# Performance work log

Hardware: AMD Instinct MI355X
Metric: run time of the kernel (lower is better)

## Reference

```python
import jax, jax.numpy as jnp
import numpy as np

B, N, D, H = 4, 2048, 512, 8
DH = D // H
EPS = 1e-6


def setup_inputs() -> dict:
    key = jax.random.key(0)
    ks = jax.random.split(key, 12)
    s = 1.0 / np.sqrt(D)
    return {
        "x": jax.random.normal(ks[0], (B, N, D), jnp.float32),
        "attn_bias": jax.random.normal(ks[1], (B, 1, N, N), jnp.float32),
        "Wq": jax.random.normal(ks[2], (D, D), jnp.float32) * s,
        "bq": jnp.zeros((D,), jnp.float32),
        "Wk": jax.random.normal(ks[3], (D, D), jnp.float32) * s,
        "bk": jnp.zeros((D,), jnp.float32),
        "Wv": jax.random.normal(ks[4], (D, D), jnp.float32) * s,
        "bv": jnp.zeros((D,), jnp.float32),
        "Wo": jax.random.normal(ks[5], (D, D), jnp.float32) * s,
        "bo": jnp.zeros((D,), jnp.float32),
        "q_gamma": jnp.ones((DH,), jnp.float32),
        "q_beta": jnp.zeros((DH,), jnp.float32),
        "k_gamma": jnp.ones((DH,), jnp.float32),
        "k_beta": jnp.zeros((DH,), jnp.float32),
    }


def _layernorm(x, gamma, beta):
    mu = jnp.mean(x, axis=-1, keepdims=True)
    var = jnp.var(x, axis=-1, keepdims=True)
    return (x - mu) * jax.lax.rsqrt(var + EPS) * gamma + beta


def reference(x, attn_bias, Wq, bq, Wk, bk, Wv, bv, Wo, bo,
              q_gamma, q_beta, k_gamma, k_beta):
    b, n, d = x.shape
    # project and split heads: (B, H, N, DH)
    def heads(W, bias):
        return (x @ W.T + bias).reshape(b, n, H, DH).transpose(0, 2, 1, 3)
    q = heads(Wq, bq)
    k = heads(Wk, bk)
    v = heads(Wv, bv)
    q = _layernorm(q, q_gamma, q_beta)
    k = _layernorm(k, k_gamma, k_beta)
    scores = jnp.einsum('bhqd,bhkd->bhqk', q, k) / np.sqrt(DH)
    scores = scores + attn_bias  # (B,1,N,N) broadcasts over heads
    attn = jax.nn.softmax(scores, axis=-1)
    out = jnp.einsum('bhqk,bhkd->bhqd', attn, v)
    out = out.transpose(0, 2, 1, 3).reshape(b, n, d)
    return out @ Wo.T + bo
```

## Files before the change

### kernel.cpp

```cpp
#include <hip/hip_runtime.h>

typedef __attribute__((ext_vector_type(8))) short short8;
typedef __attribute__((ext_vector_type(4))) float f32x4;
typedef __attribute__((ext_vector_type(4))) int i32x4;
typedef __attribute__((ext_vector_type(4))) unsigned short u16x4;
typedef __attribute__((ext_vector_type(8))) unsigned short u16x8;
typedef __attribute__((ext_vector_type(2))) unsigned int u32x2;

#define B_  4
#define N_  2048
#define D_  512
#define H_  8
#define DH_ 64
#define M_  (B_ * N_)

__device__ __forceinline__ unsigned short f2bf(float f) {
    union { float f; unsigned u; } un; un.f = f;
    unsigned r = un.u + 0x7FFFu + ((un.u >> 16) & 1u);
    return (unsigned short)(r >> 16);
}
__device__ __forceinline__ unsigned packbf(float lo, float hi) {
    union { float f; unsigned u; } a, b;
    a.f = lo; b.f = hi;
    return __builtin_amdgcn_perm(b.u + 0x8000u, a.u + 0x8000u, 0x07060302u);
}
__device__ __forceinline__ float lo16f(unsigned u) {
    union { unsigned u; float f; } un; un.u = u << 16; return un.f;
}
__device__ __forceinline__ float hi16f(unsigned u) {
    union { unsigned u; float f; } un; un.u = u & 0xFFFF0000u; return un.f;
}
__device__ __forceinline__ float exp2fast(float x) {
#if __has_builtin(__builtin_amdgcn_exp2f)
    return __builtin_amdgcn_exp2f(x);
#else
    float r; asm("v_exp_f32 %0, %1" : "=v"(r) : "v"(x)); return r;
#endif
}

typedef __attribute__((address_space(1))) const void gvoid;
typedef __attribute__((address_space(3))) void svoid;
__device__ __forceinline__ void load16_lds(const void* g, void* s) {
    __builtin_amdgcn_global_load_lds((gvoid*)g, (svoid*)s, 16, 0, 0);
}

__global__ __launch_bounds__(256) void cvt_x(const float* __restrict__ src,
                                             unsigned short* __restrict__ dst) {
    const int i = (blockIdx.x * 256 + threadIdx.x) * 4;
    f32x4 v = *(const f32x4*)(src + i);
    u16x4 o;
    o[0] = f2bf(v[0]); o[1] = f2bf(v[1]); o[2] = f2bf(v[2]); o[3] = f2bf(v[3]);
    *(u16x4*)(dst + i) = o;
}

__global__ __launch_bounds__(256) void cvt_bias(const float* __restrict__ src,
                                                unsigned short* __restrict__ dst) {
    const size_t i = ((size_t)blockIdx.x * 256 + threadIdx.x) * 8;
    const int kv = (int)(i & 2047);
    const int q  = (int)((i >> 11) & 2047);
    const int b  = (int)(i >> 22);
    const float L2E = 1.4426950408889634f;
    f32x4 v0 = *(const f32x4*)(src + i);
    f32x4 v1 = *(const f32x4*)(src + i + 4);
    u16x8 o;
    o[0] = f2bf(v0[0] * L2E); o[1] = f2bf(v0[1] * L2E);
    o[2] = f2bf(v0[2] * L2E); o[3] = f2bf(v0[3] * L2E);
    o[4] = f2bf(v1[0] * L2E); o[5] = f2bf(v1[1] * L2E);
    o[6] = f2bf(v1[2] * L2E); o[7] = f2bf(v1[3] * L2E);
    const size_t oi = ((((size_t)b * 64 + (q >> 5)) * 32 + (kv >> 6)) * 32 + (q & 31)) * 64 + (kv & 63);
    *(u16x8*)(dst + oi) = o;
}

__global__ __launch_bounds__(256) void cvt_w(const float* __restrict__ W0,
                                             const float* __restrict__ W1,
                                             const float* __restrict__ W2,
                                             const float* __restrict__ W3,
                                             unsigned short* __restrict__ dst) {
    const int sel = blockIdx.y;
    const float* src = (sel == 0) ? W0 : (sel == 1) ? W1 : (sel == 2) ? W2 : W3;
    unsigned short* d = dst + (size_t)sel * D_ * D_;
    const int i = (blockIdx.x * 256 + threadIdx.x) * 4;
    f32x4 v = *(const f32x4*)(src + i);
    u16x4 o;
    o[0] = f2bf(v[0]); o[1] = f2bf(v[1]); o[2] = f2bf(v[2]); o[3] = f2bf(v[3]);
    *(u16x4*)(d + i) = o;
}

template <bool F32OUT, bool LNF>
__global__ __launch_bounds__(256, 2) void gemm_nt(
    const unsigned short* __restrict__ A,
    const unsigned short* __restrict__ W,
    const float* __restrict__ Bv0,
    const float* __restrict__ Bv1,
    const float* __restrict__ Bv2,
    const float* __restrict__ g0, const float* __restrict__ be0,
    const float* __restrict__ g1, const float* __restrict__ be1,
    unsigned short* __restrict__ outb,
    float* __restrict__ outf)
{
    const int mt = blockIdx.x;
    const int nt = blockIdx.y;
    const int sel = nt >> 2;
    const unsigned short* Wp = W + (size_t)sel * D_ * D_;
    const float* Bv = (sel == 0) ? Bv0 : (sel == 1) ? Bv1 : Bv2;
    const int n0 = (nt & 3) * 128;

    __shared__ __align__(16) unsigned short As[128 * 32];
    __shared__ __align__(16) unsigned short Bs[128 * 32];

    const int tid = threadIdx.x;
    const int w   = tid >> 6;
    const int l   = tid & 63;
    const int l15 = l & 15;
    const int qd  = l >> 4;
    const int wr  = w >> 1;
    const int wc  = w & 1;

    int srow[2], scol[2];
#pragma unroll
    for (int c = 0; c < 2; ++c) {
        const int g   = (w * 2 + c) * 64 + l;
        const int row = g >> 2;
        srow[c] = row;
        scol[c] = ((g & 3) ^ (row & 3)) * 8;
    }

    f32x4 acc[4][4];
#pragma unroll
    for (int i = 0; i < 4; ++i)
#pragma unroll
        for (int j = 0; j < 4; ++j)
            acc[i][j] = (f32x4){0.f, 0.f, 0.f, 0.f};

    const int swz = qd ^ (l15 & 3);

    for (int k0 = 0; k0 < D_; k0 += 32) {
        __syncthreads();
#pragma unroll
        for (int c = 0; c < 2; ++c) {
            load16_lds(A  + (size_t)(mt * 128 + srow[c]) * D_ + k0 + scol[c],
                       As + (w * 2 + c) * 512);
            load16_lds(Wp + (size_t)(n0 + srow[c]) * D_ + k0 + scol[c],
                       Bs + (w * 2 + c) * 512);
        }
        __syncthreads();

        short8 af[4], bfr[4];
#pragma unroll
        for (int rt = 0; rt < 4; ++rt)
            af[rt] = *(const short8*)&As[(wr * 64 + rt * 16 + l15) * 32 + swz * 8];
#pragma unroll
        for (int ct = 0; ct < 4; ++ct)
            bfr[ct] = *(const short8*)&Bs[(wc * 64 + ct * 16 + l15) * 32 + swz * 8];
#pragma unroll
        for (int rt = 0; rt < 4; ++rt)
#pragma unroll
            for (int ct = 0; ct < 4; ++ct)
                acc[rt][ct] = __builtin_amdgcn_mfma_f32_16x16x32_bf16(
                    af[rt], bfr[ct], acc[rt][ct], 0, 0, 0);
    }

    const float* gam = (sel == 0) ? g0 : g1;
    const float* bet = (sel == 0) ? be0 : be1;
    float gv[4], bv2[4];
    if (LNF) {
#pragma unroll
        for (int ct = 0; ct < 4; ++ct) { gv[ct] = gam[ct * 16 + l15]; bv2[ct] = bet[ct * 16 + l15]; }
    }

#pragma unroll
    for (int rt = 0; rt < 4; ++rt) {
        float v[4][4];
#pragma unroll
        for (int ct = 0; ct < 4; ++ct) {
            const float bias = Bv[n0 + wc * 64 + ct * 16 + l15];
#pragma unroll
            for (int r = 0; r < 4; ++r) v[ct][r] = acc[rt][ct][r] + bias;
        }
        if (LNF && sel < 2) {
#pragma unroll
            for (int r = 0; r < 4; ++r) {
                float s  = v[0][r] + v[1][r] + v[2][r] + v[3][r];
                float s2 = v[0][r]*v[0][r] + v[1][r]*v[1][r] + v[2][r]*v[2][r] + v[3][r]*v[3][r];
#pragma unroll
                for (int o = 1; o <= 8; o <<= 1) {
                    s  += __shfl_xor(s, o);
                    s2 += __shfl_xor(s2, o);
                }
                const float mu  = s * 0.015625f;
                const float var = s2 * 0.015625f - mu * mu;
                const float rs  = rsqrtf(var + 1e-6f);
#pragma unroll
                for (int ct = 0; ct < 4; ++ct)
                    v[ct][r] = (v[ct][r] - mu) * rs * gv[ct] + bv2[ct];
            }
        }
#pragma unroll
        for (int ct = 0; ct < 4; ++ct) {
            const int col  = n0 + wc * 64 + ct * 16 + l15;
            const int row0 = mt * 128 + wr * 64 + rt * 16 + qd * 4;
#pragma unroll
            for (int r = 0; r < 4; ++r) {
                const size_t oidx = (size_t)(row0 + r) * D_ + col;
                if (F32OUT) outf[oidx] = v[ct][r];
                else        outb[(size_t)sel * M_ * D_ + oidx] = f2bf(v[ct][r]);
            }
        }
    }
}

__global__ __launch_bounds__(256) void pack_kv(
    const unsigned short* __restrict__ K, const unsigned short* __restrict__ V,
    unsigned short* __restrict__ Kt, unsigned short* __restrict__ Vt2)
{
    const int nt = blockIdx.x, b = blockIdx.y;
    const int tid = threadIdx.x;
    __shared__ __align__(16) unsigned short Vl[64][520];

#pragma unroll
    for (int i = 0; i < 16; ++i) {
        const int c = i * 256 + tid;
        const int row = c >> 6, ch = c & 63;
        const size_t srow = ((size_t)(b * N_ + nt * 64 + row)) * D_ + ch * 8;
        i32x4 kd = *(const i32x4*)(K + srow);
        const int h = ch >> 3, dc = ch & 7;
        *(i32x4*)(Kt + ((((size_t)(b * 8 + h) * 32 + nt) * 64 + row) * 64) + dc * 8) = kd;
        i32x4 vd = *(const i32x4*)(V + srow);
        *(i32x4*)&Vl[row][ch * 8] = vd;
    }
    __syncthreads();
#pragma unroll
    for (int i = 0; i < 16; ++i) {
        const int c = i * 256 + tid;
        const int h = c >> 9, r = c & 511;
        const int dh = r >> 3, kc = r & 7;
        u16x8 o;
#pragma unroll
        for (int j = 0; j < 8; ++j) o[j] = Vl[kc * 8 + j][h * 64 + dh];
        *(u16x8*)(Vt2 + ((((size_t)(b * 8 + h) * 32 + nt) * 64 + dh) * 64) + kc * 8) = o;
    }
}

__global__ __launch_bounds__(256, 2) void attn8(
    const unsigned short* __restrict__ Qm,
    const unsigned short* __restrict__ Kt,
    const unsigned short* __restrict__ Vt2,
    const unsigned short* __restrict__ Bt,
    unsigned short* __restrict__ AO)
{
    const int qt = blockIdx.x;
    const int h  = blockIdx.y;
    const int b  = blockIdx.z;
    const int w  = threadIdx.x >> 6;
    const int l  = threadIdx.x & 63;
    const int l15 = l & 15;
    const int qd  = l >> 4;
    const int q0 = qt * 128 + w * 32;

    __shared__ __align__(16) unsigned char smem[51200];
    unsigned short* PwB = (unsigned short*)(smem + 32768) + w * 32 * 72;

    int sc[2], soff[2];
#pragma unroll
    for (int i = 0; i < 2; ++i) {
        const int c = (w * 2 + i) * 64 + l;
        const int row = c >> 3, g = c & 7;
        sc[i] = c;
        soff[i] = row * 64 + (g ^ (row & 7)) * 8;
    }

    short8 qf[2][2];
#pragma unroll
    for (int ct = 0; ct < 2; ++ct)
#pragma unroll
        for (int hf = 0; hf < 2; ++hf)
            qf[ct][hf] = *(const short8*)(Qm +
                (size_t)(b * N_ + q0 + ct * 16 + l15) * D_ + h * DH_ + hf * 32 + qd * 8);

    f32x4 Ot[4][2];
#pragma unroll
    for (int rt = 0; rt < 4; ++rt)
#pragma unroll
        for (int ct = 0; ct < 2; ++ct) Ot[rt][ct] = (f32x4){0.f, 0.f, 0.f, 0.f};
    float m_i[2] = {-3.0e38f, -3.0e38f};
    float l_i[2] = {0.f, 0.f};

    const unsigned short* Ktile0 = Kt  + (((size_t)(b * 8 + h) * 32) * 64) * 64;
    const unsigned short* Vtile0 = Vt2 + (((size_t)(b * 8 + h) * 32) * 64) * 64;
    const unsigned short* Btile0 = Bt  + (((size_t)b * 64 + qt * 4 + w) * 32) * 2048;

#pragma unroll
    for (int i = 0; i < 2; ++i) {
        load16_lds(Ktile0 + soff[i], smem + sc[i] * 16);
        load16_lds(Vtile0 + soff[i], smem + 8192 + sc[i] * 16);
    }
    u32x2 brA[4][2], brB[4][2];
#pragma unroll
    for (int rt = 0; rt < 4; ++rt)
#pragma unroll
        for (int ct = 0; ct < 2; ++ct)
            brA[rt][ct] = *(const u32x2*)(Btile0 + (ct * 16 + l15) * 64 + rt * 16 + qd * 4);
    asm volatile("s_waitcnt vmcnt(0)" ::: "memory");

#define ATTN_ITER(KT, CUR, BRC, BRN) do {                                      \
    unsigned char* Kbc = smem + (CUR) * 16384;                                 \
    unsigned char* Vbc = Kbc + 8192;                                           \
    asm volatile("s_waitcnt vmcnt(8)" ::: "memory");                           \
    __builtin_amdgcn_s_barrier();                                              \
    __builtin_amdgcn_sched_barrier(0);                                         \
    if ((KT) < 31) {                                                           \
        const unsigned short* Kn = Ktile0 + (size_t)((KT) + 1) * 4096;         \
        const unsigned short* Vn = Vtile0 + (size_t)((KT) + 1) * 4096;         \
        unsigned char* KbN = smem + (((CUR) ^ 1)) * 16384;                     \
        _Pragma("unroll")                                                      \
        for (int i = 0; i < 2; ++i) {                                          \
            load16_lds(Kn + soff[i], KbN + sc[i] * 16);                        \
            load16_lds(Vn + soff[i], KbN + 8192 + sc[i] * 16);                 \
        }                                                                      \
    }                                                                          \
    asm volatile("" ::: "memory");       \
    {                                                                          \
        const unsigned short* Bn = Btile0 +                                    \
            (size_t)(((KT) < 31) ? (KT) + 1 : 31) * 2048;                      \
        _Pragma("unroll")                                                      \
        for (int rt = 0; rt < 4; ++rt)                                         \
            _Pragma("unroll")                                                  \
            for (int ct = 0; ct < 2; ++ct)                                     \
                BRN[rt][ct] = *(const u32x2*)(Bn + (ct * 16 + l15) * 64 +      \
                                              rt * 16 + qd * 4);               \
    }                                                                          \
    short8 kf[4][2];                                                           \
    _Pragma("unroll")                                                          \
    for (int rt = 0; rt < 4; ++rt) {                                           \
        const int kv = rt * 16 + l15;                                          \
        _Pragma("unroll")                                                      \
        for (int hf = 0; hf < 2; ++hf) {                                       \
            const int cidx = (hf * 4 + qd) ^ (kv & 7);                         \
            kf[rt][hf] = *(const short8*)(Kbc + kv * 128 + cidx * 16);         \
        }                                                                      \
    }                                                                          \
    f32x4 St[4][2];                                                            \
    __builtin_amdgcn_s_setprio(1);                                             \
    _Pragma("unroll")                                                          \
    for (int rt = 0; rt < 4; ++rt)                                             \
        _Pragma("unroll")                                                      \
        for (int ct = 0; ct < 2; ++ct) {                                       \
            f32x4 v = (f32x4){0.f, 0.f, 0.f, 0.f};                             \
            v = __builtin_amdgcn_mfma_f32_16x16x32_bf16(kf[rt][0], qf[ct][0], v, 0, 0, 0); \
            v = __builtin_amdgcn_mfma_f32_16x16x32_bf16(kf[rt][1], qf[ct][1], v, 0, 0, 0); \
            St[rt][ct] = v;                                                    \
        }                                                                      \
    __builtin_amdgcn_s_setprio(0);                                             \
    short8 vf[4][2];                                                           \
    _Pragma("unroll")                                                          \
    for (int rt = 0; rt < 4; ++rt) {                                           \
        const int dh = rt * 16 + l15;                                          \
        _Pragma("unroll")                                                      \
        for (int hf = 0; hf < 2; ++hf) {                                       \
            const int cidx = (hf * 4 + qd) ^ (dh & 7);                         \
            vf[rt][hf] = *(const short8*)(Vbc + dh * 128 + cidx * 16);         \
        }                                                                      \
    }                                                                          \
    _Pragma("unroll")                                                          \
    for (int ct = 0; ct < 2; ++ct) {                                           \
        float sv[4][4];                                                        \
        float mx = -3.0e38f;                                                   \
        _Pragma("unroll")                                                      \
        for (int rt = 0; rt < 4; ++rt) {                                       \
            sv[rt][0] = St[rt][ct][0] * 0.1803368801f + lo16f(BRC[rt][ct][0]); \
            sv[rt][1] = St[rt][ct][1] * 0.1803368801f + hi16f(BRC[rt][ct][0]); \
            sv[rt][2] = St[rt][ct][2] * 0.1803368801f + lo16f(BRC[rt][ct][1]); \
            sv[rt][3] = St[rt][ct][3] * 0.1803368801f + hi16f(BRC[rt][ct][1]); \
            _Pragma("unroll")                                                  \
            for (int r = 0; r < 4; ++r) mx = fmaxf(mx, sv[rt][r]);             \
        }                                                                      \
        mx = fmaxf(mx, __shfl_xor(mx, 16));                                    \
        mx = fmaxf(mx, __shfl_xor(mx, 32));                                    \
        const float mnew  = fmaxf(m_i[ct], mx);                                \
        const float alpha = exp2fast(m_i[ct] - mnew);                          \
        float rsum = 0.f;                                                      \
        _Pragma("unroll")                                                      \
        for (int rt = 0; rt < 4; ++rt) {                                       \
            const float p0 = exp2fast(sv[rt][0] - mnew);                       \
            const float p1 = exp2fast(sv[rt][1] - mnew);                       \
            const float p2 = exp2fast(sv[rt][2] - mnew);                       \
            const float p3 = exp2fast(sv[rt][3] - mnew);                       \
            rsum += (p0 + p1) + (p2 + p3);                                     \
            u32x2 pw; pw[0] = packbf(p0, p1); pw[1] = packbf(p2, p3);          \
            *(u32x2*)&PwB[(ct * 16 + l15) * 72 + rt * 16 + qd * 4] = pw;       \
        }                                                                      \
        l_i[ct] = l_i[ct] * alpha + rsum;                                      \
        m_i[ct] = mnew;                                                        \
        _Pragma("unroll")                                                      \
        for (int rt = 0; rt < 4; ++rt)                                         \
            _Pragma("unroll")                                                  \
            for (int r = 0; r < 4; ++r) Ot[rt][ct][r] *= alpha;                \
    }                                                                          \
    short8 pf[2][2];                                                           \
    _Pragma("unroll")                                                          \
    for (int ct = 0; ct < 2; ++ct)                                             \
        _Pragma("unroll")                                                      \
        for (int hf = 0; hf < 2; ++hf)                                         \
            pf[ct][hf] = *(const short8*)&PwB[(ct * 16 + l15) * 72 + hf * 32 + qd * 8]; \
    __builtin_amdgcn_s_setprio(1);                                             \
    _Pragma("unroll")                                                          \
    for (int rt = 0; rt < 4; ++rt)                                             \
        _Pragma("unroll")                                                      \
        for (int ct = 0; ct < 2; ++ct) {                                       \
            Ot[rt][ct] = __builtin_amdgcn_mfma_f32_16x16x32_bf16(vf[rt][0], pf[ct][0], Ot[rt][ct], 0, 0, 0); \
            Ot[rt][ct] = __builtin_amdgcn_mfma_f32_16x16x32_bf16(vf[rt][1], pf[ct][1], Ot[rt][ct], 0, 0, 0); \
        }                                                                      \
    __builtin_amdgcn_s_setprio(0);                                             \
} while (0)

    for (int kt2 = 0; kt2 < 16; ++kt2) {
        ATTN_ITER(kt2 * 2,     0, brA, brB);
        ATTN_ITER(kt2 * 2 + 1, 1, brB, brA);
    }
#undef ATTN_ITER

#pragma unroll
    for (int ct = 0; ct < 2; ++ct) {
        l_i[ct] += __shfl_xor(l_i[ct], 16);
        l_i[ct] += __shfl_xor(l_i[ct], 32);
        const float inv = 1.f / l_i[ct];
        const int q = q0 + ct * 16 + l15;
#pragma unroll
        for (int rt = 0; rt < 4; ++rt) {
            u16x4 ob;
#pragma unroll
            for (int r = 0; r < 4; ++r) ob[r] = f2bf(Ot[rt][ct][r] * inv);
            *(u16x4*)(AO + (size_t)(b * N_ + q) * D_ + h * DH_ + rt * 16 + qd * 4) = ob;
        }
    }
}

extern "C" void kernel_launch(void* const* d_in, const int* in_sizes, int n_in,
                              void* d_out, int out_size, void* d_ws, size_t ws_size,
                              hipStream_t stream) {
    const float* x  = (const float*)d_in[0];
    const float* ab = (const float*)d_in[1];
    const float* Wq = (const float*)d_in[2];
    const float* bq = (const float*)d_in[3];
    const float* Wk = (const float*)d_in[4];
    const float* bk = (const float*)d_in[5];
    const float* Wv = (const float*)d_in[6];
    const float* bv = (const float*)d_in[7];
    const float* Wo = (const float*)d_in[8];
    const float* bo = (const float*)d_in[9];
    const float* qg = (const float*)d_in[10];
    const float* qb = (const float*)d_in[11];
    const float* kg = (const float*)d_in[12];
    const float* kb = (const float*)d_in[13];

    unsigned short* xb  = (unsigned short*)d_ws;
    unsigned short* Wb  = xb  + (size_t)M_ * D_;
    unsigned short* Y   = Wb  + (size_t)4 * D_ * D_;
    unsigned short* Kt  = Y   + (size_t)3 * M_ * D_;
    unsigned short* Vt2 = Kt  + (size_t)M_ * D_;
    unsigned short* AO  = Vt2 + (size_t)M_ * D_;
    unsigned short* Bt  = AO  + (size_t)M_ * D_;
    float* out = (float*)d_out;

    cvt_x<<<dim3(M_ * D_ / 1024), dim3(256), 0, stream>>>(x, xb);
    cvt_w<<<dim3(D_ * D_ / 1024, 4), dim3(256), 0, stream>>>(Wq, Wk, Wv, Wo, Wb);
    cvt_bias<<<dim3((int)((size_t)B_ * N_ * N_ / 2048)), dim3(256), 0, stream>>>(ab, Bt);

    gemm_nt<false, true><<<dim3(64, 12), dim3(256), 0, stream>>>(
        xb, Wb, bq, bk, bv, qg, qb, kg, kb, Y, nullptr);

    pack_kv<<<dim3(32, 4), dim3(256), 0, stream>>>(
        Y + (size_t)M_ * D_, Y + (size_t)2 * M_ * D_, Kt, Vt2);

    attn8<<<dim3(16, 8, 4), dim3(256), 0, stream>>>(
        Y, Kt, Vt2, Bt, AO);

    gemm_nt<true, false><<<dim3(64, 4), dim3(256), 0, stream>>>(
        AO, Wb + (size_t)3 * D_ * D_, bo, bo, bo,
        nullptr, nullptr, nullptr, nullptr, nullptr, out);
}
```

Baseline: 268.9 us.

## Read fp32 attention bias directly in attention kernel, use 512-thread blocks

Removes the separate bias conversion kernel, which rescaled the B×N×N fp32 bias and wrote it to a tiled bf16 layout. The attention kernel now reads the fp32 bias row-wise and applies the log2(e) scale in registers. The attention block grows to 8 waves of 16 query rows each, so each wave keeps less register state and each lane issues one K/V LDS load per tile. The x and weight conversions are merged into one launch. The cost is that the bias is read per head at fp32 width (8x re-read across heads, twice the bytes per read) instead of once as bf16, and each K/V tile is shared across fewer query rows per wave.

```diff
diff --git a/kernel.cpp b/kernel.cpp
--- a/kernel.cpp
+++ b/kernel.cpp
@@ -24,12 +24,6 @@
     a.f = lo; b.f = hi;
     return __builtin_amdgcn_perm(b.u + 0x8000u, a.u + 0x8000u, 0x07060302u);
 }
-__device__ __forceinline__ float lo16f(unsigned u) {
-    union { unsigned u; float f; } un; un.u = u << 16; return un.f;
-}
-__device__ __forceinline__ float hi16f(unsigned u) {
-    union { unsigned u; float f; } un; un.u = u & 0xFFFF0000u; return un.f;
-}
 __device__ __forceinline__ float exp2fast(float x) {
 #if __has_builtin(__builtin_amdgcn_exp2f)
     return __builtin_amdgcn_exp2f(x);
@@ -44,46 +38,29 @@
     __builtin_amdgcn_global_load_lds((gvoid*)g, (svoid*)s, 16, 0, 0);
 }
 
-__global__ __launch_bounds__(256) void cvt_x(const float* __restrict__ src,
-                                             unsigned short* __restrict__ dst) {
-    const int i = (blockIdx.x * 256 + threadIdx.x) * 4;
+__global__ __launch_bounds__(256) void cvt_all(
+    const float* __restrict__ x,
+    const float* __restrict__ W0, const float* __restrict__ W1,
+    const float* __restrict__ W2, const float* __restrict__ W3,
+    unsigned short* __restrict__ xb, unsigned short* __restrict__ Wb) {
+    const int bx = blockIdx.x;
+    const float* src;
+    unsigned short* dst;
+    int i;
+    if (bx < 4096) {
+        src = x; dst = xb;
+        i = (bx * 256 + (int)threadIdx.x) * 4;
+    } else {
+        const int r = bx - 4096;
+        const int sel = r >> 8;
+        src = (sel == 0) ? W0 : (sel == 1) ? W1 : (sel == 2) ? W2 : W3;
+        dst = Wb + (size_t)sel * D_ * D_;
+        i = ((r & 255) * 256 + (int)threadIdx.x) * 4;
+    }
     f32x4 v = *(const f32x4*)(src + i);
     u16x4 o;
     o[0] = f2bf(v[0]); o[1] = f2bf(v[1]); o[2] = f2bf(v[2]); o[3] = f2bf(v[3]);
     *(u16x4*)(dst + i) = o;
-}
-
-__global__ __launch_bounds__(256) void cvt_bias(const float* __restrict__ src,
-                                                unsigned short* __restrict__ dst) {
-    const size_t i = ((size_t)blockIdx.x * 256 + threadIdx.x) * 8;
-    const int kv = (int)(i & 2047);
-    const int q  = (int)((i >> 11) & 2047);
-    const int b  = (int)(i >> 22);
-    const float L2E = 1.4426950408889634f;
-    f32x4 v0 = *(const f32x4*)(src + i);
-    f32x4 v1 = *(const f32x4*)(src + i + 4);
-    u16x8 o;
-    o[0] = f2bf(v0[0] * L2E); o[1] = f2bf(v0[1] * L2E);
-    o[2] = f2bf(v0[2] * L2E); o[3] = f2bf(v0[3] * L2E);
-    o[4] = f2bf(v1[0] * L2E); o[5] = f2bf(v1[1] * L2E);
-    o[6] = f2bf(v1[2] * L2E); o[7] = f2bf(v1[3] * L2E);
-    const size_t oi = ((((size_t)b * 64 + (q >> 5)) * 32 + (kv >> 6)) * 32 + (q & 31)) * 64 + (kv & 63);
-    *(u16x8*)(dst + oi) = o;
-}
-
-__global__ __launch_bounds__(256) void cvt_w(const float* __restrict__ W0,
-                                             const float* __restrict__ W1,
-                                             const float* __restrict__ W2,
-                                             const float* __restrict__ W3,
-                                             unsigned short* __restrict__ dst) {
-    const int sel = blockIdx.y;
-    const float* src = (sel == 0) ? W0 : (sel == 1) ? W1 : (sel == 2) ? W2 : W3;
-    unsigned short* d = dst + (size_t)sel * D_ * D_;
-    const int i = (blockIdx.x * 256 + threadIdx.x) * 4;
-    f32x4 v = *(const f32x4*)(src + i);
-    u16x4 o;
-    o[0] = f2bf(v[0]); o[1] = f2bf(v[1]); o[2] = f2bf(v[2]); o[3] = f2bf(v[3]);
-    *(u16x4*)(d + i) = o;
 }
 
 template <bool F32OUT, bool LNF>
@@ -241,11 +218,11 @@
     }
 }
 
-__global__ __launch_bounds__(256, 2) void attn8(
+__global__ __launch_bounds__(512, 4) void attn9(
     const unsigned short* __restrict__ Qm,
     const unsigned short* __restrict__ Kt,
     const unsigned short* __restrict__ Vt2,
-    const unsigned short* __restrict__ Bt,
+    const float* __restrict__ Bias,
     unsigned short* __restrict__ AO)
 {
     const int qt = blockIdx.x;
@@ -255,79 +232,60 @@
     const int l  = threadIdx.x & 63;
     const int l15 = l & 15;
     const int qd  = l >> 4;
-    const int q0 = qt * 128 + w * 32;
+    const int q0 = qt * 128 + w * 16;
 
     __shared__ __align__(16) unsigned char smem[51200];
-    unsigned short* PwB = (unsigned short*)(smem + 32768) + w * 32 * 72;
-
-    int sc[2], soff[2];
-#pragma unroll
-    for (int i = 0; i < 2; ++i) {
-        const int c = (w * 2 + i) * 64 + l;
-        const int row = c >> 3, g = c & 7;
-        sc[i] = c;
-        soff[i] = row * 64 + (g ^ (row & 7)) * 8;
-    }
-
-    short8 qf[2][2];
-#pragma unroll
-    for (int ct = 0; ct < 2; ++ct)
-#pragma unroll
-        for (int hf = 0; hf < 2; ++hf)
-            qf[ct][hf] = *(const short8*)(Qm +
-                (size_t)(b * N_ + q0 + ct * 16 + l15) * D_ + h * DH_ + hf * 32 + qd * 8);
-
-    f32x4 Ot[4][2];
-#pragma unroll
-    for (int rt = 0; rt < 4; ++rt)
-#pragma unroll
-        for (int ct = 0; ct < 2; ++ct) Ot[rt][ct] = (f32x4){0.f, 0.f, 0.f, 0.f};
-    float m_i[2] = {-3.0e38f, -3.0e38f};
-    float l_i[2] = {0.f, 0.f};
+    unsigned short* PwB = (unsigned short*)(smem + 32768) + w * 16 * 72;
+
+    const int c    = w * 64 + l;
+    const int srow = c >> 3;
+    const int sg   = (c & 7) ^ (srow & 7);
+    const int soff = srow * 64 + sg * 8;
+    const int sc16 = c * 16;
+
+    short8 qf[2];
+#pragma unroll
+    for (int hf = 0; hf < 2; ++hf)
+        qf[hf] = *(const short8*)(Qm +
+            (size_t)(b * N_ + q0 + l15) * D_ + h * DH_ + hf * 32 + qd * 8);
+
+    f32x4 Ot[4];
+#pragma unroll
+    for (int rt = 0; rt < 4; ++rt) Ot[rt] = (f32x4){0.f, 0.f, 0.f, 0.f};
+    float m_i = -3.0e38f;
+    float l_i = 0.f;
 
     const unsigned short* Ktile0 = Kt  + (((size_t)(b * 8 + h) * 32) * 64) * 64;
     const unsigned short* Vtile0 = Vt2 + (((size_t)(b * 8 + h) * 32) * 64) * 64;
-    const unsigned short* Btile0 = Bt  + (((size_t)b * 64 + qt * 4 + w) * 32) * 2048;
-
-#pragma unroll
-    for (int i = 0; i < 2; ++i) {
-        load16_lds(Ktile0 + soff[i], smem + sc[i] * 16);
-        load16_lds(Vtile0 + soff[i], smem + 8192 + sc[i] * 16);
-    }
-    u32x2 brA[4][2], brB[4][2];
+    const float* biasQ = Bias + ((size_t)b * N_ + q0 + l15) * N_;
+
+    load16_lds(Ktile0 + soff, smem + sc16);
+    load16_lds(Vtile0 + soff, smem + 8192 + sc16);
+    f32x4 brA[4], brB[4];
 #pragma unroll
     for (int rt = 0; rt < 4; ++rt)
-#pragma unroll
-        for (int ct = 0; ct < 2; ++ct)
-            brA[rt][ct] = *(const u32x2*)(Btile0 + (ct * 16 + l15) * 64 + rt * 16 + qd * 4);
+        brA[rt] = *(const f32x4*)(biasQ + rt * 16 + qd * 4);
     asm volatile("s_waitcnt vmcnt(0)" ::: "memory");
 
 #define ATTN_ITER(KT, CUR, BRC, BRN) do {                                      \
     unsigned char* Kbc = smem + (CUR) * 16384;                                 \
     unsigned char* Vbc = Kbc + 8192;                                           \
-    asm volatile("s_waitcnt vmcnt(8)" ::: "memory");                           \
+    asm volatile("s_waitcnt vmcnt(4)" ::: "memory");                           \
     __builtin_amdgcn_s_barrier();                                              \
     __builtin_amdgcn_sched_barrier(0);                                         \
     if ((KT) < 31) {                                                           \
         const unsigned short* Kn = Ktile0 + (size_t)((KT) + 1) * 4096;         \
         const unsigned short* Vn = Vtile0 + (size_t)((KT) + 1) * 4096;         \
         unsigned char* KbN = smem + (((CUR) ^ 1)) * 16384;                     \
-        _Pragma("unroll")                                                      \
-        for (int i = 0; i < 2; ++i) {                                          \
-            load16_lds(Kn + soff[i], KbN + sc[i] * 16);                        \
-            load16_lds(Vn + soff[i], KbN + 8192 + sc[i] * 16);                 \
-        }                                                                      \
+        load16_lds(Kn + soff, KbN + sc16);                                     \
+        load16_lds(Vn + soff, KbN + 8192 + sc16);                              \
     }                                                                          \
     asm volatile("" ::: "memory");       \
     {                                                                          \
-        const unsigned short* Bn = Btile0 +                                    \
-            (size_t)(((KT) < 31) ? (KT) + 1 : 31) * 2048;                      \
+        const float* Bn = biasQ + (size_t)(((KT) < 31) ? (KT) + 1 : 31) * 64;  \
         _Pragma("unroll")                                                      \
         for (int rt = 0; rt < 4; ++rt)                                         \
-            _Pragma("unroll")                                                  \
-            for (int ct = 0; ct < 2; ++ct)                                     \
-                BRN[rt][ct] = *(const u32x2*)(Bn + (ct * 16 + l15) * 64 +      \
-                                              rt * 16 + qd * 4);               \
+            BRN[rt] = *(const f32x4*)(Bn + rt * 16 + qd * 4);                  \
     }                                                                          \
     short8 kf[4][2];                                                           \
     _Pragma("unroll")                                                          \
@@ -339,17 +297,15 @@
             kf[rt][hf] = *(const short8*)(Kbc + kv * 128 + cidx * 16);         \
         }                                                                      \
     }                                                                          \
-    f32x4 St[4][2];                                                            \
+    f32x4 St[4];                                                               \
     __builtin_amdgcn_s_setprio(1);                                             \
     _Pragma("unroll")                                                          \
-    for (int rt = 0; rt < 4; ++rt)                                             \
-        _Pragma("unroll")                                                      \
-        for (int ct = 0; ct < 2; ++ct) {                                       \
-            f32x4 v = (f32x4){0.f, 0.f, 0.f, 0.f};                             \
-            v = __builtin_amdgcn_mfma_f32_16x16x32_bf16(kf[rt][0], qf[ct][0], v, 0, 0, 0); \
-            v = __builtin_amdgcn_mfma_f32_16x16x32_bf16(kf[rt][1], qf[ct][1], v, 0, 0, 0); \
-            St[rt][ct] = v;                                                    \
-        }                                                                      \
+    for (int rt = 0; rt < 4; ++rt) {                                           \
+        f32x4 v = (f32x4){0.f, 0.f, 0.f, 0.f};                                 \
+        v = __builtin_amdgcn_mfma_f32_16x16x32_bf16(kf[rt][0], qf[0], v, 0, 0, 0); \
+        v = __builtin_amdgcn_mfma_f32_16x16x32_bf16(kf[rt][1], qf[1], v, 0, 0, 0); \
+        St[rt] = v;                                                            \
+    }                                                                          \
     __builtin_amdgcn_s_setprio(0);                                             \
     short8 vf[4][2];                                                           \
     _Pragma("unroll")                                                          \
@@ -361,23 +317,22 @@
             vf[rt][hf] = *(const short8*)(Vbc + dh * 128 + cidx * 16);         \
         }                                                                      \
     }                                                                          \
-    _Pragma("unroll")                                                          \
-    for (int ct = 0; ct < 2; ++ct) {                                           \
+    {                                                                          \
         float sv[4][4];                                                        \
         float mx = -3.0e38f;                                                   \
         _Pragma("unroll")                                                      \
         for (int rt = 0; rt < 4; ++rt) {                                       \
-            sv[rt][0] = St[rt][ct][0] * 0.1803368801f + lo16f(BRC[rt][ct][0]); \
-            sv[rt][1] = St[rt][ct][1] * 0.1803368801f + hi16f(BRC[rt][ct][0]); \
-            sv[rt][2] = St[rt][ct][2] * 0.1803368801f + lo16f(BRC[rt][ct][1]); \
-            sv[rt][3] = St[rt][ct][3] * 0.1803368801f + hi16f(BRC[rt][ct][1]); \
             _Pragma("unroll")                                                  \
-            for (int r = 0; r < 4; ++r) mx = fmaxf(mx, sv[rt][r]);             \
+            for (int r = 0; r < 4; ++r) {                                      \
+                sv[rt][r] = St[rt][r] * 0.1803368801f +                        \
+                            BRC[rt][r] * 1.4426950408889634f;                  \
+                mx = fmaxf(mx, sv[rt][r]);                                     \
+            }                                                                  \
         }                                                                      \
         mx = fmaxf(mx, __shfl_xor(mx, 16));                                    \
         mx = fmaxf(mx, __shfl_xor(mx, 32));                                    \
-        const float mnew  = fmaxf(m_i[ct], mx);                                \
-        const float alpha = exp2fast(m_i[ct] - mnew);                          \
+        const float mnew  = fmaxf(m_i, mx);                                    \
+        const float alpha = exp2fast(m_i - mnew);                              \
         float rsum = 0.f;                                                      \
         _Pragma("unroll")                                                      \
         for (int rt = 0; rt < 4; ++rt) {                                       \
@@ -387,29 +342,25 @@
             const float p3 = exp2fast(sv[rt][3] - mnew);                       \
             rsum += (p0 + p1) + (p2 + p3);                                     \
             u32x2 pw; pw[0] = packbf(p0, p1); pw[1] = packbf(p2, p3);          \
-            *(u32x2*)&PwB[(ct * 16 + l15) * 72 + rt * 16 + qd * 4] = pw;       \
+            *(u32x2*)&PwB[l15 * 72 + rt * 16 + qd * 4] = pw;                   \
         }                                                                      \
-        l_i[ct] = l_i[ct] * alpha + rsum;                                      \
-        m_i[ct] = mnew;                                                        \
+        l_i = l_i * alpha + rsum;                                              \
+        m_i = mnew;                                                            \
         _Pragma("unroll")                                                      \
         for (int rt = 0; rt < 4; ++rt)                                         \
             _Pragma("unroll")                                                  \
-            for (int r = 0; r < 4; ++r) Ot[rt][ct][r] *= alpha;                \
-    }                                                                          \
-    short8 pf[2][2];                                                           \
+            for (int r = 0; r < 4; ++r) Ot[rt][r] *= alpha;                    \
+    }                                                                          \
+    short8 pf[2];                                                              \
     _Pragma("unroll")                                                          \
-    for (int ct = 0; ct < 2; ++ct)                                             \
-        _Pragma("unroll")                                                      \
-        for (int hf = 0; hf < 2; ++hf)                                         \
-            pf[ct][hf] = *(const short8*)&PwB[(ct * 16 + l15) * 72 + hf * 32 + qd * 8]; \
+    for (int hf = 0; hf < 2; ++hf)                                             \
+        pf[hf] = *(const short8*)&PwB[l15 * 72 + hf * 32 + qd * 8];            \
     __builtin_amdgcn_s_setprio(1);                                             \
     _Pragma("unroll")                                                          \
-    for (int rt = 0; rt < 4; ++rt)                                             \
-        _Pragma("unroll")                                                      \
-        for (int ct = 0; ct < 2; ++ct) {                                       \
-            Ot[rt][ct] = __builtin_amdgcn_mfma_f32_16x16x32_bf16(vf[rt][0], pf[ct][0], Ot[rt][ct], 0, 0, 0); \
-            Ot[rt][ct] = __builtin_amdgcn_mfma_f32_16x16x32_bf16(vf[rt][1], pf[ct][1], Ot[rt][ct], 0, 0, 0); \
-        }                                                                      \
+    for (int rt = 0; rt < 4; ++rt) {                                           \
+        Ot[rt] = __builtin_amdgcn_mfma_f32_16x16x32_bf16(vf[rt][0], pf[0], Ot[rt], 0, 0, 0); \
+        Ot[rt] = __builtin_amdgcn_mfma_f32_16x16x32_bf16(vf[rt][1], pf[1], Ot[rt], 0, 0, 0); \
+    }                                                                          \
     __builtin_amdgcn_s_setprio(0);                                             \
 } while (0)
 
@@ -419,19 +370,16 @@
     }
 #undef ATTN_ITER
 
-#pragma unroll
-    for (int ct = 0; ct < 2; ++ct) {
-        l_i[ct] += __shfl_xor(l_i[ct], 16);
-        l_i[ct] += __shfl_xor(l_i[ct], 32);
-        const float inv = 1.f / l_i[ct];
-        const int q = q0 + ct * 16 + l15;
-#pragma unroll
-        for (int rt = 0; rt < 4; ++rt) {
-            u16x4 ob;
-#pragma unroll
-            for (int r = 0; r < 4; ++r) ob[r] = f2bf(Ot[rt][ct][r] * inv);
-            *(u16x4*)(AO + (size_t)(b * N_ + q) * D_ + h * DH_ + rt * 16 + qd * 4) = ob;
-        }
+    l_i += __shfl_xor(l_i, 16);
+    l_i += __shfl_xor(l_i, 32);
+    const float inv = 1.f / l_i;
+    const int q = q0 + l15;
+#pragma unroll
+    for (int rt = 0; rt < 4; ++rt) {
+        u16x4 ob;
+#pragma unroll
+        for (int r = 0; r < 4; ++r) ob[r] = f2bf(Ot[rt][r] * inv);
+        *(u16x4*)(AO + (size_t)(b * N_ + q) * D_ + h * DH_ + rt * 16 + qd * 4) = ob;
     }
 }
 
@@ -459,12 +407,9 @@
     unsigned short* Kt  = Y   + (size_t)3 * M_ * D_;
     unsigned short* Vt2 = Kt  + (size_t)M_ * D_;
     unsigned short* AO  = Vt2 + (size_t)M_ * D_;
-    unsigned short* Bt  = AO  + (size_t)M_ * D_;
     float* out = (float*)d_out;
 
-    cvt_x<<<dim3(M_ * D_ / 1024), dim3(256), 0, stream>>>(x, xb);
-    cvt_w<<<dim3(D_ * D_ / 1024, 4), dim3(256), 0, stream>>>(Wq, Wk, Wv, Wo, Wb);
-    cvt_bias<<<dim3((int)((size_t)B_ * N_ * N_ / 2048)), dim3(256), 0, stream>>>(ab, Bt);
+    cvt_all<<<dim3(5120), dim3(256), 0, stream>>>(x, Wq, Wk, Wv, Wo, xb, Wb);
 
     gemm_nt<false, true><<<dim3(64, 12), dim3(256), 0, stream>>>(
         xb, Wb, bq, bk, bv, qg, qb, kg, kb, Y, nullptr);
@@ -472,8 +417,8 @@
     pack_kv<<<dim3(32, 4), dim3(256), 0, stream>>>(
         Y + (size_t)M_ * D_, Y + (size_t)2 * M_ * D_, Kt, Vt2);
 
-    attn8<<<dim3(16, 8, 4), dim3(256), 0, stream>>>(
-        Y, Kt, Vt2, Bt, AO);
+    attn9<<<dim3(16, 8, 4), dim3(512), 0, stream>>>(
+        Y, Kt, Vt2, ab, AO);
 
     gemm_nt<true, false><<<dim3(64, 4), dim3(256), 0, stream>>>(
         AO, Wb + (size_t)3 * D_ * D_, bo, bo, bo,
```

Result: faster. 254.8 us (-5.3%).
